# Performance work log

Hardware: AMD Instinct MI355X
Metric: run time of the kernel (lower is better)

The kernel has to match this reference:

```python
import jax, jax.numpy as jnp
import numpy as np

B, S, T, H, D = 4, 128, 128, 256, 3


def setup_inputs() -> dict:
    key = jax.random.key(0)
    ks = jax.random.split(key, 10)
    s = 1.0 / np.sqrt(H).astype(np.float32)
    return {
        "src": jax.random.normal(ks[0], (B, S, H), jnp.float32),
        "trg": jax.random.normal(ks[1], (B, T, H), jnp.float32),
        "Wx_ih": jax.random.normal(ks[2], (D, H, H), jnp.float32) * s,
        "Wx_hh": jax.random.normal(ks[3], (D, H, H), jnp.float32) * s,
        "bx_ih": jax.random.normal(ks[4], (D, H), jnp.float32) * s,
        "bx_hh": jax.random.normal(ks[5], (D, H), jnp.float32) * s,
        "Wy_ih": jax.random.normal(ks[6], (D, H, H), jnp.float32) * s,
        "Wy_hh": jax.random.normal(ks[7], (D, H, H), jnp.float32) * s,
        "by_ih": jax.random.normal(ks[8], (D, H), jnp.float32) * s,
        "by_hh": jax.random.normal(ks[9], (D, H), jnp.float32) * s,
    }


def _grid_rnn(src, trg, Wx_ih, Wx_hh, bx_ih, bx_hh, Wy_ih, Wy_hh, by_ih, by_hh):
    dt = src.dtype
    hx = hy = None
    for d in range(D):
        if d == 0:
            xin = jnp.broadcast_to(src[:, :, None, :], (B, S, T, H))  # x_t(i,j)=src[i]
            yin = jnp.broadcast_to(trg[:, None, :, :], (B, S, T, H))  # y_t(i,j)=trg[j]
        else:
            xin, yin = hx, hy  # outputs of previous depth

        # ---- h_x: recurrence over rows i; state_x(i,j) = h_x(i-1, j-1),
        # with j==0 reading index -2 (Python wraparound) = h_x(i-1, T-1) -> jnp.roll.
        Wih, Whh, bih, bhh = Wx_ih[d], Wx_hh[d], bx_ih[d], bx_hh[d]

        def step_x(carry, x_i, Wih=Wih, Whh=Whh, bih=bih, bhh=bhh):
            state = jnp.roll(carry, 1, axis=1)  # [B,T,H]: state[j] = carry[j-1]
            h = jnp.tanh(x_i @ Wih.T + bih + state @ Whh.T + bhh)
            return h, h

        _, hx = jax.lax.scan(step_x, jnp.zeros((B, T, H), dt), jnp.swapaxes(xin, 0, 1))
        hx = jnp.swapaxes(hx, 0, 1)  # [B,S,T,H]

        # ---- h_y: recurrence over columns j; state_y(i,j) = h_y(i, j-1); rows independent.
        Wihy, Whhy, bihy, bhhy = Wy_ih[d], Wy_hh[d], by_ih[d], by_hh[d]

        def step_y(carry, y_j, Wih=Wihy, Whh=Whhy, bih=bihy, bhh=bhhy):
            h = jnp.tanh(y_j @ Wih.T + bih + carry @ Whh.T + bhh)
            return h, h

        _, hy = jax.lax.scan(step_y, jnp.zeros((B, S, H), dt), jnp.moveaxis(yin, 2, 0))
        hy = jnp.moveaxis(hy, 0, 2)  # [B,S,T,H]

    # final-depth output grid: slot 2j = h_x, slot 2j+1 = h_y
    return jnp.stack([hx, hy], axis=-2)  # [B,S,T,2,H]


def reference(src, trg, Wx_ih, Wx_hh, bx_ih, bx_hh, Wy_ih, Wy_hh, by_ih, by_hh):
    return _grid_rnn(src, trg, Wx_ih, Wx_hh, bx_ih, bx_hh, Wy_ih, Wy_hh, by_ih, by_hh)
```

## Files before the change

kernel.cpp:

```cpp
#include <hip/hip_runtime.h>


#define SS 128
#define TT 128
#define HH 256
#define GRID_ELEMS ((size_t)4 * 128 * 128 * 256)

typedef _Float16 half8 __attribute__((ext_vector_type(8)));
typedef float float4v __attribute__((ext_vector_type(4)));
typedef float float2v __attribute__((ext_vector_type(2)));

__device__ __forceinline__ float fast_tanh(float x) {
    float e = __expf(2.0f * x);
    return 1.0f - 2.0f / (e + 1.0f);
}

__device__ __forceinline__ unsigned short f2hbits(float x) {
    _Float16 h = (_Float16)x;
    return __builtin_bit_cast(unsigned short, h);
}

__device__ __forceinline__ float sel4(float4v v, int q) {
    float a = (q & 1) ? v[1] : v[0];
    float b = (q & 1) ? v[3] : v[2];
    return (q & 2) ? b : a;
}

__device__ __forceinline__ void lds_barrier() {
    asm volatile("s_waitcnt lgkmcnt(0)" ::: "memory");
    __builtin_amdgcn_s_barrier();
}

__device__ __forceinline__ half8 ldfrag_f32(const float* rowp, int k) {
    const float4v u0 = *(const float4v*)(rowp + k);
    const float4v u1 = *(const float4v*)(rowp + k + 4);
    half8 v;
#pragma unroll
    for (int e = 0; e < 4; ++e) { v[e] = (_Float16)u0[e]; v[4 + e] = (_Float16)u1[e]; }
    return v;
}

extern "C" __global__ void __launch_bounds__(512, 2)
grid_gemm0(const float* __restrict__ src, const float* __restrict__ trg,
           const float* __restrict__ Wx_ih, const float* __restrict__ Wy_ih,
           const float* __restrict__ bx_ih, const float* __restrict__ bx_hh,
           const float* __restrict__ by_ih, const float* __restrict__ by_hh,
           float* __restrict__ P0)
{
    __shared__ half8 aT[2048];

    const int tid  = threadIdx.x;
    const int lane = tid & 63;
    const int wv   = tid >> 6;
    const int quad = lane >> 4;
    const int l15  = lane & 15;

    const int bx    = blockIdx.x;
    const int dir   = bx >> 3;
    const int mtile = bx & 7;

    const float* Wih = dir ? Wy_ih : Wx_ih;
    const float* bih = dir ? by_ih : bx_ih;
    const float* bhh = dir ? by_hh : bx_hh;

    const int n_0 = (wv << 5) + l15;
    const int n_1 = n_0 + 16;

    half8 B0[8], B1[8];
    {
        const float* r0 = Wih + (size_t)n_0 * HH;
        const float* r1 = Wih + (size_t)n_1 * HH;
#pragma unroll
        for (int f = 0; f < 8; ++f) {
            const int k = (f << 5) + (quad << 3);
            B0[f] = ldfrag_f32(r0, k);
            B1[f] = ldfrag_f32(r1, k);
        }
    }
    const float bias0 = bih[n_0] + bhh[n_0];
    const float bias1 = bih[n_1] + bhh[n_1];

#pragma unroll
    for (int i = 0; i < 4; ++i) {
        const int c  = (tid << 2) + i;
        const int r  = c >> 5;
        const int kc = c & 31;
        const int R  = (mtile << 6) + r;
        const int b  = R >> 7, ii = R & 127;
        const float* row = (dir ? trg : src) + (size_t)((b << 7) + ii) * HH + (kc << 3);
        const float4v u0 = *(const float4v*)(row);
        const float4v u1 = *(const float4v*)(row + 4);
        half8 v;
#pragma unroll
        for (int e = 0; e < 4; ++e) { v[e] = (_Float16)u0[e]; v[4 + e] = (_Float16)u1[e]; }
        aT[((r >> 4) << 9) + ((kc >> 2) << 6) + ((kc & 3) << 4) + (r & 15)] = v;
    }
    __syncthreads();

#pragma unroll
    for (int msub = 0; msub < 4; ++msub) {
        half8 af[8];
#pragma unroll
        for (int f = 0; f < 8; ++f)
            af[f] = aT[(msub << 9) + (f << 6) + (quad << 4) + l15];

        float4v c0 = {bias0, bias0, bias0, bias0};
        float4v c1 = {bias1, bias1, bias1, bias1};
#pragma unroll
        for (int f = 0; f < 8; ++f) {
            c0 = __builtin_amdgcn_mfma_f32_16x16x32_f16(af[f], B0[f], c0, 0, 0, 0);
            c1 = __builtin_amdgcn_mfma_f32_16x16x32_f16(af[f], B1[f], c1, 0, 0, 0);
        }
#pragma unroll
        for (int r = 0; r < 4; ++r) {
            const int row = (msub << 4) + (quad << 2) + r;
            float* p = P0 + (size_t)dir * 131072 + (size_t)((mtile << 6) + row) * HH;
            p[n_0] = c0[r];
            p[n_1] = c1[r];
        }
    }
}

template <int DI>
__device__ __forceinline__ void rnn2f_body(
    const float* __restrict__ Wx_hh, const float* __restrict__ Wy_hh,
    const float* __restrict__ Wx_ih, const float* __restrict__ Wy_ih,
    const float* __restrict__ bx_ih, const float* __restrict__ bx_hh,
    const float* __restrict__ by_ih, const float* __restrict__ by_hh,
    float* __restrict__ out, const float* __restrict__ P0)
{
    __shared__ half8 aH[8][128];

    const int tid  = threadIdx.x;
    const int lane = tid & 63;
    const int wv   = tid >> 6;
    const int quad = lane >> 4;
    const int l15  = lane & 15;
    const int lrow = lane & 3;

    const int bid  = blockIdx.x;
    const int isY  = bid >= 128;
    const int g0   = isY ? bid - 128 : bid;
    const int b    = g0 >> 5;
    const int c0   = (g0 & 31) << 2;
    const int slot = isY;

    const float* Whh  = (isY ? Wy_hh : Wx_hh) + (size_t)DI * HH * HH;
    const float* WihN = (isY ? Wy_ih : Wx_ih) + (size_t)(DI + 1) * HH * HH;
    const float* bihN = (isY ? by_ih : bx_ih) + (DI + 1) * HH;
    const float* bhhN = (isY ? by_hh : bx_hh) + (DI + 1) * HH;

    const int n_0 = (wv << 5) + l15;
    const int n_1 = n_0 + 16;

    half8 Bhh0[8], Bhh1[8], BN0[8], BN1[8];
    {
        const float* h0p = Whh  + (size_t)n_0 * HH;
        const float* h1p = Whh  + (size_t)n_1 * HH;
        const float* i0p = WihN + (size_t)n_0 * HH;
        const float* i1p = WihN + (size_t)n_1 * HH;
#pragma unroll
        for (int f = 0; f < 8; ++f) {
            const int k = (f << 5) + (quad << 3);
            Bhh0[f] = ldfrag_f32(h0p, k);
            Bhh1[f] = ldfrag_f32(h1p, k);
            BN0[f]  = ldfrag_f32(i0p, k);
            BN1[f]  = ldfrag_f32(i1p, k);
        }
    }
    const float biasN0 = bihN[n_0] + bhhN[n_0];
    const float biasN1 = bihN[n_1] + bhhN[n_1];

    float pA[4], pB[4];
    int rj = isY ? 0 : ((c0 + quad) & 127);
    const float* rp;
    if constexpr (DI == 0) {
        rp = P0 + (size_t)isY * 131072 + (size_t)b * 128 * HH;
    } else {
        rp = out + (isY ? ((size_t)(b * SS + c0 + quad) * TT)
                        : ((size_t)b * SS * TT + rj)) * 2 * HH
                 + (size_t)slot * HH;
    }
    auto rbump = [&]() {
        if constexpr (DI == 0) { rp += HH; }
        else if (isY)          { rp += 2 * HH; }
        else { rp += (size_t)(rj == 127 ? 1 : 129) * 2 * HH; rj = (rj + 1) & 127; }
    };
#pragma unroll
    for (int u = 0; u < 4; ++u) { pA[u] = rp[n_0]; pB[u] = rp[n_1]; rbump(); }

    auto store_group = [&](int t4, const float4v& v0, const float4v& v1) {
        const int t = t4 + quad;
#pragma unroll
        for (int r = 0; r < 4; ++r) {
            const int ch = c0 + r;
            const size_t cell = isY ? ((size_t)(b * SS + ch) * TT + t)
                                    : ((size_t)(b * SS + t) * TT + ((ch + t) & 127));
            float* p = out + cell * 2 * HH + (size_t)slot * HH;
            p[n_0] = v0[r];
            p[n_1] = v1[r];
        }
    };

    if (tid < 128) {
        half8 z;
#pragma unroll
        for (int e = 0; e < 8; ++e) z[e] = (_Float16)0.f;
        aH[0][tid] = z;
    }
    __syncthreads();

    const int hi  = l15 >> 3;
    const int lo3 = l15 & 7;

    float4v pn0 = {0.f, 0.f, 0.f, 0.f}, pn1 = {0.f, 0.f, 0.f, 0.f};
    float4v st0 = {0.f, 0.f, 0.f, 0.f}, st1 = {0.f, 0.f, 0.f, 0.f};

    for (int g = 0; g < 32; ++g) {
#pragma unroll
        for (int u = 0; u < 4; ++u) {
            const int s = (g << 2) + u;

            if (u == 0 && g >= 2) store_group(((g - 2) << 2), st0, st1);

            const float pAu = pA[u], pBu = pB[u];
            if (s + 4 < 128) { pA[u] = rp[n_0]; pB[u] = rp[n_1]; rbump(); }

            const half8* hb = aH[s & 7];
            half8 ahr[8];
#pragma unroll
            for (int f = 0; f < 8; ++f)
                ahr[f] = hb[(f << 4) + (quad << 2) + lrow];

            float4v a0a = {0.f,0.f,0.f,0.f}, a0b = {0.f,0.f,0.f,0.f};
            float4v a1a = {0.f,0.f,0.f,0.f}, a1b = {0.f,0.f,0.f,0.f};
            __builtin_amdgcn_s_setprio(1);
#pragma unroll
            for (int f = 0; f < 4; ++f) {
                a0a = __builtin_amdgcn_mfma_f32_16x16x32_f16(ahr[f],     Bhh0[f],     a0a, 0, 0, 0);
                a1a = __builtin_amdgcn_mfma_f32_16x16x32_f16(ahr[f],     Bhh1[f],     a1a, 0, 0, 0);
                a0b = __builtin_amdgcn_mfma_f32_16x16x32_f16(ahr[f + 4], Bhh0[f + 4], a0b, 0, 0, 0);
                a1b = __builtin_amdgcn_mfma_f32_16x16x32_f16(ahr[f + 4], Bhh1[f + 4], a1b, 0, 0, 0);
            }
            __builtin_amdgcn_s_setprio(0);

            const float h0 = fast_tanh(sel4(a0a, quad) + sel4(a0b, quad) + pAu);
            const float h1 = fast_tanh(sel4(a1a, quad) + sel4(a1b, quad) + pBu);
            unsigned short* aHu = (unsigned short*)aH[(s + 1) & 7];
            aHu[(((wv << 4) + (hi << 2) + quad) << 3) + lo3]       = f2hbits(h0);
            aHu[(((wv << 4) + ((2 + hi) << 2) + quad) << 3) + lo3] = f2hbits(h1);

            __builtin_amdgcn_sched_barrier(0);

            if (g >= 1) {
                if (u == 0) {
                    pn0 = float4v{biasN0, biasN0, biasN0, biasN0};
                    pn1 = float4v{biasN1, biasN1, biasN1, biasN1};
                }
                const half8* ib = aH[((g << 2) - 3 + (l15 >> 2)) & 7];
#pragma unroll
                for (int ff = 0; ff < 2; ++ff) {
                    const int f = (u << 1) + ff;
                    const half8 af = ib[(f << 4) + (quad << 2) + (l15 & 3)];
                    pn0 = __builtin_amdgcn_mfma_f32_16x16x32_f16(af, BN0[f], pn0, 0, 0, 0);
                    pn1 = __builtin_amdgcn_mfma_f32_16x16x32_f16(af, BN1[f], pn1, 0, 0, 0);
                }
                if (u == 3) { st0 = pn0; st1 = pn1; }
            }

            lds_barrier();
            __builtin_amdgcn_sched_barrier(0);
        }
    }

    store_group((30 << 2), st0, st1);
    {
        float4v p0 = {biasN0, biasN0, biasN0, biasN0};
        float4v p1 = {biasN1, biasN1, biasN1, biasN1};
        const half8* ib = aH[(5 + (l15 >> 2)) & 7];
#pragma unroll
        for (int f = 0; f < 8; ++f) {
            const half8 af = ib[(f << 4) + (quad << 2) + (l15 & 3)];
            p0 = __builtin_amdgcn_mfma_f32_16x16x32_f16(af, BN0[f], p0, 0, 0, 0);
            p1 = __builtin_amdgcn_mfma_f32_16x16x32_f16(af, BN1[f], p1, 0, 0, 0);
        }
        store_group((31 << 2), p0, p1);
    }
}

extern "C" __global__ void __launch_bounds__(512, 1)
grid_rnn2f_d0(const float* __restrict__ Wx_hh, const float* __restrict__ Wy_hh,
              const float* __restrict__ Wx_ih, const float* __restrict__ Wy_ih,
              const float* __restrict__ bx_ih, const float* __restrict__ bx_hh,
              const float* __restrict__ by_ih, const float* __restrict__ by_hh,
              float* __restrict__ out, const float* __restrict__ P0)
{ rnn2f_body<0>(Wx_hh, Wy_hh, Wx_ih, Wy_ih, bx_ih, bx_hh, by_ih, by_hh, out, P0); }

extern "C" __global__ void __launch_bounds__(512, 1)
grid_rnn2f_d1(const float* __restrict__ Wx_hh, const float* __restrict__ Wy_hh,
              const float* __restrict__ Wx_ih, const float* __restrict__ Wy_ih,
              const float* __restrict__ bx_ih, const float* __restrict__ bx_hh,
              const float* __restrict__ by_ih, const float* __restrict__ by_hh,
              float* __restrict__ out, const float* __restrict__ P0)
{ rnn2f_body<1>(Wx_hh, Wy_hh, Wx_ih, Wy_ih, bx_ih, bx_hh, by_ih, by_hh, out, P0); }

extern "C" __global__ void __launch_bounds__(512, 2)
grid_rnn2_last(const float* __restrict__ Wx_hh, const float* __restrict__ Wy_hh,
               float* __restrict__ out)
{
    __shared__ half8 aH[2][128];

    const int tid  = threadIdx.x;
    const int lane = tid & 63;
    const int wv   = tid >> 6;
    const int quad = lane >> 4;
    const int l15  = lane & 15;
    const int lrow = lane & 3;

    const int bid  = blockIdx.x;
    const int isY  = bid >= 128;
    const int g    = isY ? bid - 128 : bid;
    const int b    = g >> 5;
    const int c0   = (g & 31) << 2;
    const int slot = isY;

    const float* Whh = (isY ? Wy_hh : Wx_hh) + (size_t)2 * HH * HH;

    const int n_0 = (wv << 5) + l15;
    const int n_1 = n_0 + 16;

    half8 Bhh0[8], Bhh1[8];
    {
        const float* r0 = Whh + (size_t)n_0 * HH;
        const float* r1 = Whh + (size_t)n_1 * HH;
#pragma unroll
        for (int f = 0; f < 8; ++f) {
            const int k = (f << 5) + (quad << 3);
            Bhh0[f] = ldfrag_f32(r0, k);
            Bhh1[f] = ldfrag_f32(r1, k);
        }
    }

    float pA[4], pB[4];
    int rj = isY ? 0 : ((c0 + quad) & 127);
    const float* rp = out + (isY ? ((size_t)(b * SS + c0 + quad) * TT)
                                 : ((size_t)b * SS * TT + rj)) * 2 * HH
                          + (size_t)slot * HH;
    auto rbump = [&]() {
        if (isY) { rp += 2 * HH; }
        else { rp += (size_t)(rj == 127 ? 1 : 129) * 2 * HH; rj = (rj + 1) & 127; }
    };
#pragma unroll
    for (int u = 0; u < 4; ++u) { pA[u] = rp[n_0]; pB[u] = rp[n_1]; rbump(); }

    const int sm = tid >> 7;
    const int kk = (tid & 127) << 1;
    int sj = isY ? 0 : ((c0 + sm) & 127);
    float* sp = out + (isY ? ((size_t)(b * SS + c0 + sm) * TT)
                           : ((size_t)b * SS * TT + sj)) * 2 * HH
                    + (size_t)slot * HH + kk;
    const int rb32 = ((((kk >> 3) << 2) + sm) << 3 | (kk & 7)) >> 1;

    auto store_spread = [&](int bufi) {
        const unsigned int* a32 = (const unsigned int*)aH[bufi];
        const unsigned int w = a32[rb32];
        const _Float16 lo = __builtin_bit_cast(_Float16, (unsigned short)(w & 0xffff));
        const _Float16 hv = __builtin_bit_cast(_Float16, (unsigned short)(w >> 16));
        float2v t; t[0] = (float)lo; t[1] = (float)hv;
        *(float2v*)sp = t;
        if (isY) { sp += 2 * HH; }
        else { sp += (size_t)(sj == 127 ? 1 : 129) * 2 * HH; sj = (sj + 1) & 127; }
    };

    if (tid < 128) {
        half8 z;
#pragma unroll
        for (int e = 0; e < 8; ++e) z[e] = (_Float16)0.f;
        aH[0][tid] = z;
    }
    __syncthreads();

    const int hi  = l15 >> 3;
    const int lo3 = l15 & 7;

    int buf = 0;
    for (int s4 = 0; s4 < 128; s4 += 4) {
#pragma unroll
        for (int u = 0; u < 4; ++u) {
            const int s = s4 + u;

            if (s > 0) store_spread(buf);

            const float pAu = pA[u], pBu = pB[u];
            if (s + 4 < 128) { pA[u] = rp[n_0]; pB[u] = rp[n_1]; rbump(); }

            half8 ahr[8];
#pragma unroll
            for (int f = 0; f < 8; ++f)
                ahr[f] = aH[buf][(f << 4) + (quad << 2) + lrow];

            float4v a0a = {0.f,0.f,0.f,0.f}, a0b = {0.f,0.f,0.f,0.f};
            float4v a1a = {0.f,0.f,0.f,0.f}, a1b = {0.f,0.f,0.f,0.f};
            __builtin_amdgcn_s_setprio(1);
#pragma unroll
            for (int f = 0; f < 4; ++f) {
                a0a = __builtin_amdgcn_mfma_f32_16x16x32_f16(ahr[f],     Bhh0[f],     a0a, 0, 0, 0);
                a1a = __builtin_amdgcn_mfma_f32_16x16x32_f16(ahr[f],     Bhh1[f],     a1a, 0, 0, 0);
                a0b = __builtin_amdgcn_mfma_f32_16x16x32_f16(ahr[f + 4], Bhh0[f + 4], a0b, 0, 0, 0);
                a1b = __builtin_amdgcn_mfma_f32_16x16x32_f16(ahr[f + 4], Bhh1[f + 4], a1b, 0, 0, 0);
            }
            __builtin_amdgcn_s_setprio(0);

            const float h0 = fast_tanh(sel4(a0a, quad) + sel4(a0b, quad) + pAu);
            const float h1 = fast_tanh(sel4(a1a, quad) + sel4(a1b, quad) + pBu);
            unsigned short* aHu = (unsigned short*)aH[buf ^ 1];
            aHu[(((wv << 4) + (hi << 2) + quad) << 3) + lo3]       = f2hbits(h0);
            aHu[(((wv << 4) + ((2 + hi) << 2) + quad) << 3) + lo3] = f2hbits(h1);

            lds_barrier();
            __builtin_amdgcn_sched_barrier(0);
            buf ^= 1;
        }
    }

    store_spread(buf);
}

template <int DI>
__device__ __forceinline__ void grid_rnn_body_v1(
    const float* __restrict__ src, const float* __restrict__ trg,
    const float* __restrict__ Wx_ih, const float* __restrict__ Wx_hh,
    const float* __restrict__ bx_ih, const float* __restrict__ bx_hh,
    const float* __restrict__ Wy_ih, const float* __restrict__ Wy_hh,
    const float* __restrict__ by_ih, const float* __restrict__ by_hh,
    float* __restrict__ out)
{
    __shared__ half8 aX[2][128];
    __shared__ half8 aH[2][128];

    const int tid  = threadIdx.x;
    const int lane = tid & 63;
    const int wv   = tid >> 6;
    const int quad = lane >> 4;
    const int l15  = lane & 15;

    const int bid  = blockIdx.x;
    const int isY  = bid >= 128;
    const int g    = isY ? bid - 128 : bid;
    const int b    = g >> 5;
    const int c0   = (g & 31) << 2;
    const int slot = isY;

    const float* Wih = (isY ? Wy_ih : Wx_ih) + (size_t)DI * HH * HH;
    const float* Whh = (isY ? Wy_hh : Wx_hh) + (size_t)DI * HH * HH;
    const float* bih = (isY ? by_ih : bx_ih) + DI * HH;
    const float* bhh = (isY ? by_hh : bx_hh) + DI * HH;

    const int n_0 = (wv << 5) + l15;
    const int n_1 = n_0 + 16;

    half8 Bih0[8], Bih1[8], Bhh0[8], Bhh1[8];
    {
        const float* r0i = Wih + (size_t)n_0 * HH;
        const float* r1i = Wih + (size_t)n_1 * HH;
        const float* r0h = Whh + (size_t)n_0 * HH;
        const float* r1h = Whh + (size_t)n_1 * HH;
#pragma unroll
        for (int f = 0; f < 8; ++f) {
            const int k = (f << 5) + (quad << 3);
            Bih0[f] = ldfrag_f32(r0i, k);
            Bih1[f] = ldfrag_f32(r1i, k);
            Bhh0[f] = ldfrag_f32(r0h, k);
            Bhh1[f] = ldfrag_f32(r1h, k);
        }
    }
    const float bias0 = bih[n_0] + bhh[n_0];
    const float bias1 = bih[n_1] + bhh[n_1];

    const int sact = (tid < 128);
    const int cm   = tid & 3;
    const int ck0  = (tid >> 2) << 3;
    const int chc  = c0 + cm;

    auto stage_now = [&](int sn) -> half8 {
        const int i = isY ? chc : sn;
        const int j = isY ? sn : ((chc + sn) & 127);
        const size_t cell = (size_t)(b * SS + i) * TT + j;
        half8 v;
        if constexpr (DI == 0) {
            const float* row = isY ? (trg + (size_t)(b * TT + j) * HH)
                                   : (src + (size_t)(b * SS + i) * HH);
            const float4v u0 = *(const float4v*)(row + ck0);
            const float4v u1 = *(const float4v*)(row + ck0 + 4);
#pragma unroll
            for (int e = 0; e < 4; ++e) { v[e] = (_Float16)u0[e]; v[4 + e] = (_Float16)u1[e]; }
        } else {
            const float* row = out + cell * 2 * HH + (size_t)slot * HH + ck0;
            const float4v u0 = *(const float4v*)(row);
            const float4v u1 = *(const float4v*)(row + 4);
#pragma unroll
            for (int e = 0; e < 4; ++e) { v[e] = (_Float16)u0[e]; v[4 + e] = (_Float16)u1[e]; }
        }
        return v;
    };

    auto store_h = [&](int sp, int bufi) {
        const half8 v = aH[bufi][tid];
        const int i = isY ? chc : sp;
        const int j = isY ? sp : ((chc + sp) & 127);
        const size_t cell = (size_t)(b * SS + i) * TT + j;
        float* p = out + cell * 2 * HH + (size_t)slot * HH + ck0;
        float4v u0, u1;
#pragma unroll
        for (int e = 0; e < 4; ++e) { u0[e] = (float)v[e]; u1[e] = (float)v[4 + e]; }
        *(float4v*)p = u0;
        *(float4v*)(p + 4) = u1;
    };

    if (sact) {
        half8 z;
#pragma unroll
        for (int e = 0; e < 8; ++e) z[e] = (_Float16)0.f;
        aH[0][tid] = z;
        aX[0][tid] = stage_now(0);
    }
    __syncthreads();

    const int lrow = lane & 3;

    int buf = 0;
    for (int s = 0; s < 128; ++s) {
        if (s > 0 && sact) store_h(s - 1, buf);
        if (sact) {
            int t = s + 1; if (t > 127) t = 127;
            aX[buf ^ 1][tid] = stage_now(t);
        }

        half8 axr[8], ahr[8];
#pragma unroll
        for (int f = 0; f < 8; ++f) {
            const int e = (f << 4) + (quad << 2) + lrow;
            axr[f] = aX[buf][e];
            ahr[f] = aH[buf][e];
        }

        float4v ax0 = {bias0, bias0, bias0, bias0};
        float4v ax1 = {bias1, bias1, bias1, bias1};
        float4v ah0 = {0.f, 0.f, 0.f, 0.f};
        float4v ah1 = {0.f, 0.f, 0.f, 0.f};
#pragma unroll
        for (int f = 0; f < 8; ++f) {
            ax0 = __builtin_amdgcn_mfma_f32_16x16x32_f16(axr[f], Bih0[f], ax0, 0, 0, 0);
            ax1 = __builtin_amdgcn_mfma_f32_16x16x32_f16(axr[f], Bih1[f], ax1, 0, 0, 0);
            ah0 = __builtin_amdgcn_mfma_f32_16x16x32_f16(ahr[f], Bhh0[f], ah0, 0, 0, 0);
            ah1 = __builtin_amdgcn_mfma_f32_16x16x32_f16(ahr[f], Bhh1[f], ah1, 0, 0, 0);
        }

        if (quad == 0) {
            unsigned short* aHu = (unsigned short*)aH[buf ^ 1];
            const int lo3 = lane & 7;
            const int hi  = lane >> 3;
#pragma unroll
            for (int r = 0; r < 4; ++r) {
                const float h0 = fast_tanh(ax0[r] + ah0[r]);
                const float h1 = fast_tanh(ax1[r] + ah1[r]);
                aHu[(wv << 7) + (hi << 5) + (r << 3) + lo3]       = f2hbits(h0);
                aHu[(wv << 7) + ((2 + hi) << 5) + (r << 3) + lo3] = f2hbits(h1);
            }
        }

        lds_barrier();
        buf ^= 1;
    }

    if (sact) store_h(127, buf);
}

extern "C" __global__ void __launch_bounds__(512, 2)
grid_rnn_v1_d0(const float* __restrict__ src, const float* __restrict__ trg,
               const float* __restrict__ Wx_ih, const float* __restrict__ Wx_hh,
               const float* __restrict__ bx_ih, const float* __restrict__ bx_hh,
               const float* __restrict__ Wy_ih, const float* __restrict__ Wy_hh,
               const float* __restrict__ by_ih, const float* __restrict__ by_hh,
               float* __restrict__ out)
{ grid_rnn_body_v1<0>(src, trg, Wx_ih, Wx_hh, bx_ih, bx_hh, Wy_ih, Wy_hh, by_ih, by_hh, out); }

extern "C" __global__ void __launch_bounds__(512, 2)
grid_rnn_v1_d1(const float* __restrict__ src, const float* __restrict__ trg,
               const float* __restrict__ Wx_ih, const float* __restrict__ Wx_hh,
               const float* __restrict__ bx_ih, const float* __restrict__ bx_hh,
               const float* __restrict__ Wy_ih, const float* __restrict__ Wy_hh,
               const float* __restrict__ by_ih, const float* __restrict__ by_hh,
               float* __restrict__ out)
{ grid_rnn_body_v1<1>(src, trg, Wx_ih, Wx_hh, bx_ih, bx_hh, Wy_ih, Wy_hh, by_ih, by_hh, out); }

extern "C" __global__ void __launch_bounds__(512, 2)
grid_rnn_v1_d2(const float* __restrict__ src, const float* __restrict__ trg,
               const float* __restrict__ Wx_ih, const float* __restrict__ Wx_hh,
               const float* __restrict__ bx_ih, const float* __restrict__ bx_hh,
               const float* __restrict__ Wy_ih, const float* __restrict__ Wy_hh,
               const float* __restrict__ by_ih, const float* __restrict__ by_hh,
               float* __restrict__ out)
{ grid_rnn_body_v1<2>(src, trg, Wx_ih, Wx_hh, bx_ih, bx_hh, Wy_ih, Wy_hh, by_ih, by_hh, out); }

extern "C" void kernel_launch(void* const* d_in, const int* in_sizes, int n_in,
                              void* d_out, int out_size, void* d_ws, size_t ws_size,
                              hipStream_t stream) {
    const float* src   = (const float*)d_in[0];
    const float* trg   = (const float*)d_in[1];
    const float* Wx_ih = (const float*)d_in[2];
    const float* Wx_hh = (const float*)d_in[3];
    const float* bx_ih = (const float*)d_in[4];
    const float* bx_hh = (const float*)d_in[5];
    const float* Wy_ih = (const float*)d_in[6];
    const float* Wy_hh = (const float*)d_in[7];
    const float* by_ih = (const float*)d_in[8];
    const float* by_hh = (const float*)d_in[9];
    float* out = (float*)d_out;
    float* wsf = (float*)d_ws;

    const size_t needP0 = (size_t)2 * 131072 * sizeof(float);

    if (ws_size >= needP0) {
        hipLaunchKernelGGL(grid_gemm0, dim3(16), dim3(512), 0, stream,
                           src, trg, Wx_ih, Wy_ih, bx_ih, bx_hh, by_ih, by_hh, wsf);
        hipLaunchKernelGGL(grid_rnn2f_d0, dim3(256), dim3(512), 0, stream,
                           Wx_hh, Wy_hh, Wx_ih, Wy_ih, bx_ih, bx_hh, by_ih, by_hh,
                           out, (const float*)wsf);
        hipLaunchKernelGGL(grid_rnn2f_d1, dim3(256), dim3(512), 0, stream,
                           Wx_hh, Wy_hh, Wx_ih, Wy_ih, bx_ih, bx_hh, by_ih, by_hh,
                           out, (const float*)wsf);
        hipLaunchKernelGGL(grid_rnn2_last, dim3(256), dim3(512), 0, stream,
                           Wx_hh, Wy_hh, out);
    } else {
        hipLaunchKernelGGL(grid_rnn_v1_d0, dim3(256), dim3(512), 0, stream,
                           src, trg, Wx_ih, Wx_hh, bx_ih, bx_hh,
                           Wy_ih, Wy_hh, by_ih, by_hh, out);
        hipLaunchKernelGGL(grid_rnn_v1_d1, dim3(256), dim3(512), 0, stream,
                           src, trg, Wx_ih, Wx_hh, bx_ih, bx_hh,
                           Wy_ih, Wy_hh, by_ih, by_hh, out);
        hipLaunchKernelGGL(grid_rnn_v1_d2, dim3(256), dim3(512), 0, stream,
                           src, trg, Wx_ih, Wx_hh, bx_ih, bx_hh,
                           Wy_ih, Wy_hh, by_ih, by_hh, out);
    }
}
```

Measured before the change: 418.4 us.

## Fuse four phase kernels into one cooperative persistent kernel with grid syncs

Merges the input GEMM, the two fused depth phases and the last-depth recurrence into a single cooperative kernel that uses grid.sync between phases. The aim is to remove three kernel launch gaps and the tail and ramp-up between dependent launches. In exchange the fused kernel needs more registers and LDS, since the phases' shared arrays may all be allocated at once, and it uses launch bounds of one block per CU. If the cooperative launch fails it falls back to the four separate launches.

```diff
diff --git a/kernel.cpp b/kernel.cpp
--- a/kernel.cpp
+++ b/kernel.cpp
@@ -1,4 +1,5 @@
 #include <hip/hip_runtime.h>
+#include <hip/hip_cooperative_groups.h>
 
 
 #define SS 128
@@ -6,6 +7,8 @@
 #define HH 256
 #define GRID_ELEMS ((size_t)4 * 128 * 128 * 256)
 
+namespace cg = cooperative_groups;
+
 typedef _Float16 half8 __attribute__((ext_vector_type(8)));
 typedef float float4v __attribute__((ext_vector_type(4)));
 typedef float float2v __attribute__((ext_vector_type(2)));
@@ -40,12 +43,12 @@
     return v;
 }
 
-extern "C" __global__ void __launch_bounds__(512, 2)
-grid_gemm0(const float* __restrict__ src, const float* __restrict__ trg,
-           const float* __restrict__ Wx_ih, const float* __restrict__ Wy_ih,
-           const float* __restrict__ bx_ih, const float* __restrict__ bx_hh,
-           const float* __restrict__ by_ih, const float* __restrict__ by_hh,
-           float* __restrict__ P0)
+__device__ __forceinline__ void gemm0_phase(
+    const float* __restrict__ src, const float* __restrict__ trg,
+    const float* __restrict__ Wx_ih, const float* __restrict__ Wy_ih,
+    const float* __restrict__ bx_ih, const float* __restrict__ bx_hh,
+    const float* __restrict__ by_ih, const float* __restrict__ by_hh,
+    float* __restrict__ P0, int bx)
 {
     __shared__ half8 aT[2048];
 
@@ -55,7 +58,6 @@
     const int quad = lane >> 4;
     const int l15  = lane & 15;
 
-    const int bx    = blockIdx.x;
     const int dir   = bx >> 3;
     const int mtile = bx & 7;
 
@@ -122,12 +124,12 @@
 }
 
 template <int DI>
-__device__ __forceinline__ void rnn2f_body(
+__device__ __forceinline__ void rnn2f_phase(
     const float* __restrict__ Wx_hh, const float* __restrict__ Wy_hh,
     const float* __restrict__ Wx_ih, const float* __restrict__ Wy_ih,
     const float* __restrict__ bx_ih, const float* __restrict__ bx_hh,
     const float* __restrict__ by_ih, const float* __restrict__ by_hh,
-    float* __restrict__ out, const float* __restrict__ P0)
+    float* __restrict__ out, const float* __restrict__ P0, int bid)
 {
     __shared__ half8 aH[8][128];
 
@@ -138,7 +140,6 @@
     const int l15  = lane & 15;
     const int lrow = lane & 3;
 
-    const int bid  = blockIdx.x;
     const int isY  = bid >= 128;
     const int g0   = isY ? bid - 128 : bid;
     const int b    = g0 >> 5;
@@ -288,25 +289,9 @@
     }
 }
 
-extern "C" __global__ void __launch_bounds__(512, 1)
-grid_rnn2f_d0(const float* __restrict__ Wx_hh, const float* __restrict__ Wy_hh,
-              const float* __restrict__ Wx_ih, const float* __restrict__ Wy_ih,
-              const float* __restrict__ bx_ih, const float* __restrict__ bx_hh,
-              const float* __restrict__ by_ih, const float* __restrict__ by_hh,
-              float* __restrict__ out, const float* __restrict__ P0)
-{ rnn2f_body<0>(Wx_hh, Wy_hh, Wx_ih, Wy_ih, bx_ih, bx_hh, by_ih, by_hh, out, P0); }
-
-extern "C" __global__ void __launch_bounds__(512, 1)
-grid_rnn2f_d1(const float* __restrict__ Wx_hh, const float* __restrict__ Wy_hh,
-              const float* __restrict__ Wx_ih, const float* __restrict__ Wy_ih,
-              const float* __restrict__ bx_ih, const float* __restrict__ bx_hh,
-              const float* __restrict__ by_ih, const float* __restrict__ by_hh,
-              float* __restrict__ out, const float* __restrict__ P0)
-{ rnn2f_body<1>(Wx_hh, Wy_hh, Wx_ih, Wy_ih, bx_ih, bx_hh, by_ih, by_hh, out, P0); }
-
-extern "C" __global__ void __launch_bounds__(512, 2)
-grid_rnn2_last(const float* __restrict__ Wx_hh, const float* __restrict__ Wy_hh,
-               float* __restrict__ out)
+__device__ __forceinline__ void rnn2_last_phase(
+    const float* __restrict__ Wx_hh, const float* __restrict__ Wy_hh,
+    float* __restrict__ out, int bid)
 {
     __shared__ half8 aH[2][128];
 
@@ -317,7 +302,6 @@
     const int l15  = lane & 15;
     const int lrow = lane & 3;
 
-    const int bid  = blockIdx.x;
     const int isY  = bid >= 128;
     const int g    = isY ? bid - 128 : bid;
     const int b    = g >> 5;
@@ -425,6 +409,64 @@
 
     store_spread(buf);
 }
+
+extern "C" __global__ void __launch_bounds__(512, 1)
+grnn_all(const float* __restrict__ src, const float* __restrict__ trg,
+         const float* __restrict__ Wx_ih, const float* __restrict__ Wx_hh,
+         const float* __restrict__ bx_ih, const float* __restrict__ bx_hh,
+         const float* __restrict__ Wy_ih, const float* __restrict__ Wy_hh,
+         const float* __restrict__ by_ih, const float* __restrict__ by_hh,
+         float* __restrict__ out, float* __restrict__ P0)
+{
+    const int bid = blockIdx.x;
+    cg::grid_group grid = cg::this_grid();
+
+    if (bid < 16)
+        gemm0_phase(src, trg, Wx_ih, Wy_ih, bx_ih, bx_hh, by_ih, by_hh, P0, bid);
+    __threadfence();
+    grid.sync();
+
+    rnn2f_phase<0>(Wx_hh, Wy_hh, Wx_ih, Wy_ih, bx_ih, bx_hh, by_ih, by_hh,
+                   out, P0, bid);
+    __threadfence();
+    grid.sync();
+
+    rnn2f_phase<1>(Wx_hh, Wy_hh, Wx_ih, Wy_ih, bx_ih, bx_hh, by_ih, by_hh,
+                   out, P0, bid);
+    __threadfence();
+    grid.sync();
+
+    rnn2_last_phase(Wx_hh, Wy_hh, out, bid);
+}
+
+extern "C" __global__ void __launch_bounds__(512, 2)
+grid_gemm0(const float* __restrict__ src, const float* __restrict__ trg,
+           const float* __restrict__ Wx_ih, const float* __restrict__ Wy_ih,
+           const float* __restrict__ bx_ih, const float* __restrict__ bx_hh,
+           const float* __restrict__ by_ih, const float* __restrict__ by_hh,
+           float* __restrict__ P0)
+{ gemm0_phase(src, trg, Wx_ih, Wy_ih, bx_ih, bx_hh, by_ih, by_hh, P0, blockIdx.x); }
+
+extern "C" __global__ void __launch_bounds__(512, 1)
+grid_rnn2f_d0(const float* __restrict__ Wx_hh, const float* __restrict__ Wy_hh,
+              const float* __restrict__ Wx_ih, const float* __restrict__ Wy_ih,
+              const float* __restrict__ bx_ih, const float* __restrict__ bx_hh,
+              const float* __restrict__ by_ih, const float* __restrict__ by_hh,
+              float* __restrict__ out, const float* __restrict__ P0)
+{ rnn2f_phase<0>(Wx_hh, Wy_hh, Wx_ih, Wy_ih, bx_ih, bx_hh, by_ih, by_hh, out, P0, blockIdx.x); }
+
+extern "C" __global__ void __launch_bounds__(512, 1)
+grid_rnn2f_d1(const float* __restrict__ Wx_hh, const float* __restrict__ Wy_hh,
+              const float* __restrict__ Wx_ih, const float* __restrict__ Wy_ih,
+              const float* __restrict__ bx_ih, const float* __restrict__ bx_hh,
+              const float* __restrict__ by_ih, const float* __restrict__ by_hh,
+              float* __restrict__ out, const float* __restrict__ P0)
+{ rnn2f_phase<1>(Wx_hh, Wy_hh, Wx_ih, Wy_ih, bx_ih, bx_hh, by_ih, by_hh, out, P0, blockIdx.x); }
+
+extern "C" __global__ void __launch_bounds__(512, 2)
+grid_rnn2_last(const float* __restrict__ Wx_hh, const float* __restrict__ Wy_hh,
+               float* __restrict__ out)
+{ rnn2_last_phase(Wx_hh, Wy_hh, out, blockIdx.x); }
 
 template <int DI>
 __device__ __forceinline__ void grid_rnn_body_v1(
@@ -622,16 +664,26 @@
     const size_t needP0 = (size_t)2 * 131072 * sizeof(float);
 
     if (ws_size >= needP0) {
-        hipLaunchKernelGGL(grid_gemm0, dim3(16), dim3(512), 0, stream,
-                           src, trg, Wx_ih, Wy_ih, bx_ih, bx_hh, by_ih, by_hh, wsf);
-        hipLaunchKernelGGL(grid_rnn2f_d0, dim3(256), dim3(512), 0, stream,
-                           Wx_hh, Wy_hh, Wx_ih, Wy_ih, bx_ih, bx_hh, by_ih, by_hh,
-                           out, (const float*)wsf);
-        hipLaunchKernelGGL(grid_rnn2f_d1, dim3(256), dim3(512), 0, stream,
-                           Wx_hh, Wy_hh, Wx_ih, Wy_ih, bx_ih, bx_hh, by_ih, by_hh,
-                           out, (const float*)wsf);
-        hipLaunchKernelGGL(grid_rnn2_last, dim3(256), dim3(512), 0, stream,
-                           Wx_hh, Wy_hh, out);
+        void* args[] = {
+            (void*)&src, (void*)&trg,
+            (void*)&Wx_ih, (void*)&Wx_hh, (void*)&bx_ih, (void*)&bx_hh,
+            (void*)&Wy_ih, (void*)&Wy_hh, (void*)&by_ih, (void*)&by_hh,
+            (void*)&out, (void*)&wsf
+        };
+        hipError_t err = hipLaunchCooperativeKernel(
+            (void*)grnn_all, dim3(256), dim3(512), args, 0, stream);
+        if (err != hipSuccess) {
+            hipLaunchKernelGGL(grid_gemm0, dim3(16), dim3(512), 0, stream,
+                               src, trg, Wx_ih, Wy_ih, bx_ih, bx_hh, by_ih, by_hh, wsf);
+            hipLaunchKernelGGL(grid_rnn2f_d0, dim3(256), dim3(512), 0, stream,
+                               Wx_hh, Wy_hh, Wx_ih, Wy_ih, bx_ih, bx_hh, by_ih, by_hh,
+                               out, (const float*)wsf);
+            hipLaunchKernelGGL(grid_rnn2f_d1, dim3(256), dim3(512), 0, stream,
+                               Wx_hh, Wy_hh, Wx_ih, Wy_ih, bx_ih, bx_hh, by_ih, by_hh,
+                               out, (const float*)wsf);
+            hipLaunchKernelGGL(grid_rnn2_last, dim3(256), dim3(512), 0, stream,
+                               Wx_hh, Wy_hh, out);
+        }
     } else {
         hipLaunchKernelGGL(grid_rnn_v1_d0, dim3(256), dim3(512), 0, stream,
                            src, trg, Wx_ih, Wx_hh, bx_ih, bx_hh,
```

Result: slower. 681.1 us (+62.8%).
